# Kernel optimization log

Measured on AMD Instinct MI355X. Metric: run time of the kernel, lower is better.

## Reference

```python
import jax, jax.numpy as jnp
import numpy as np

CAUSAL = True


def setup_inputs() -> dict:
    key = jax.random.key(0)
    k1, k2, k3 = jax.random.split(key, 3)
    B, H, T, D = 2, 16, 2048, 64
    q = jax.random.normal(k1, (B, H, T, D), dtype=jnp.float32)
    k = jax.random.normal(k2, (B, H, T, D), dtype=jnp.float32)
    v = jax.random.normal(k3, (B, H, T, D), dtype=jnp.float32)
    return {"q": q, "k": k, "v": v}


def reference(q, k, v):
    # q,k,v: [B,H,T,D]
    d = q.shape[-1]
    scale = d ** -0.5
    dots = jnp.einsum('bhid,bhjd->bhij', q, k) * scale  # [B,H,T,T]
    if CAUSAL:
        t = q.shape[2]
        mask = jnp.triu(jnp.ones((t, t), dtype=bool), k=1)  # True above diagonal
        dots = jnp.where(mask, -jnp.inf, dots)
    attn = jax.nn.softmax(dots, axis=-1)
    # torch.einsum('bhjd,bhij->bhid', v, attn) == attn @ v
    return jnp.einsum('bhij,bhjd->bhid', attn, v)
```

## Files before the change

### kernel.cpp

```cpp
#include <hip/hip_runtime.h>
#include <hip/hip_bf16.h>

typedef unsigned short u16;
typedef unsigned int u32;
typedef __bf16 bf16x8 __attribute__((ext_vector_type(8)));
typedef short s16x4 __attribute__((ext_vector_type(4)));
typedef short s16x8 __attribute__((ext_vector_type(8)));
typedef float floatx4 __attribute__((ext_vector_type(4)));

#define T_SEQ 2048
#define HDIM 64
#define NBH 32

static __device__ __forceinline__ u16 f2b_rne(float x) {
    union { float f; u32 u; } c; c.f = x;
    u32 u = c.u;
    return (u16)((u + 0x7fffu + ((u >> 16) & 1u)) >> 16);
}
static __device__ __forceinline__ u16 f2b_trunc(float x) {
    union { float f; u32 u; } c; c.f = x;
    return (u16)(c.u >> 16);
}

#define GLOAD_LDS16(gp, lp)                                                      \
    __builtin_amdgcn_global_load_lds(                                            \
        (const __attribute__((address_space(1))) u32*)(gp),                      \
        (__attribute__((address_space(3))) u32*)(lp), 16, 0, 0)

__global__ __launch_bounds__(256) void prep(const float* __restrict__ k,
                                            const float* __restrict__ v,
                                            u16* __restrict__ kb,
                                            u16* __restrict__ vt) {
    __shared__ u16 tile[64][68];
    const int bh = blockIdx.y, t0 = blockIdx.x * 64;
    const int tid = threadIdx.x;

    const float* ksrc = k + ((size_t)bh * T_SEQ + t0) * HDIM;
    u16* kdst = kb + ((size_t)bh * T_SEQ + t0) * HDIM;
#pragma unroll
    for (int p = 0; p < 4; p++) {
        int idx = p * 256 + tid;
        float4 f = ((const float4*)ksrc)[idx];
        ushort4 o;
        o.x = f2b_rne(f.x); o.y = f2b_rne(f.y); o.z = f2b_rne(f.z); o.w = f2b_rne(f.w);
        ((ushort4*)kdst)[idx] = o;
    }

    const float* vsrc = v + ((size_t)bh * T_SEQ + t0) * HDIM;
#pragma unroll
    for (int p = 0; p < 4; p++) {
        int idx = p * 256 + tid;
        int r = idx >> 4, c4 = (idx & 15) * 4;
        float4 f = *(const float4*)(vsrc + r * HDIM + c4);
        tile[c4 + 0][r] = f2b_rne(f.x);
        tile[c4 + 1][r] = f2b_rne(f.y);
        tile[c4 + 2][r] = f2b_rne(f.z);
        tile[c4 + 3][r] = f2b_rne(f.w);
    }
    __syncthreads();
    u16* dst = vt + (size_t)bh * HDIM * T_SEQ + t0;
#pragma unroll
    for (int p = 0; p < 4; p++) {
        int idx = p * 256 + tid;
        int d = idx >> 4, c4 = (idx & 15) * 4;
        int t = c4 >> 4, qg = (c4 >> 2) & 3;
        int pos = qg * 16 + (t >> 1) * 8 + (t & 1) * 4;
        *(ushort4*)(dst + (size_t)d * T_SEQ + pos) = *(ushort4*)(&tile[d][c4]);
    }
}

__global__ __launch_bounds__(256, 4) void fattn(const float* __restrict__ q,
                                                const u16* __restrict__ kb,
                                                const u16* __restrict__ vtb,
                                                float* __restrict__ out) {
    __shared__ __align__(16) u16 Kl[2][64 * 64];
    __shared__ __align__(16) u16 Vl[2][64 * 64];

    const int bh = blockIdx.x;
    const int s = blockIdx.y;
    const int qt = (s & 8) ? (s ^ 7) : s;
    const int tid = threadIdx.x;
    const int wave = tid >> 6, lane = tid & 63;
    const int l15 = lane & 15, quad = lane >> 4;

    const float* qp = q + (size_t)bh * T_SEQ * HDIM;
    const u16* kp = kb + (size_t)bh * T_SEQ * HDIM;
    const u16* vp = vtb + (size_t)bh * HDIM * T_SEQ;

    const int qrow_base = qt * 64 + wave * 16;

    const int srow = wave * 8 + (lane >> 3);
    const int slot = lane & 7;
    const u16* kg0 = kp + srow * HDIM + (slot ^ (srow & 7)) * 8;
    const int vs = (slot - srow) & 7;
    const u16* vg0 = vp + (size_t)srow * T_SEQ + vs * 8;
    const u16* vg1 = vp + (size_t)(srow + 32) * T_SEQ + vs * 8;

    auto stage = [&](int j, int buf) {
        const u16* ks = kg0 + j * 64 * HDIM;
        u16* Kd = &Kl[buf][wave * 512];
        GLOAD_LDS16(ks, Kd);
        GLOAD_LDS16(ks + 32 * HDIM, Kd + 2048);
        u16* Vd = &Vl[buf][wave * 512];
        GLOAD_LDS16(vg0 + j * 64, Vd);
        GLOAD_LDS16(vg1 + j * 64, Vd + 2048);
    };

    stage(0, 0);

    const float SL2E = 0.125f * 1.44269504088896f;
    bf16x8 qf[2];
    {
        const float* qrow = qp + (size_t)(qrow_base + l15) * HDIM;
#pragma unroll
        for (int kc = 0; kc < 2; kc++) {
            const float4* p4 = (const float4*)(qrow + kc * 32 + quad * 8);
            float4 fa = p4[0], fb = p4[1];
            union { bf16x8 v; u16 s[8]; } cv;
            cv.s[0] = f2b_rne(fa.x * SL2E); cv.s[1] = f2b_rne(fa.y * SL2E);
            cv.s[2] = f2b_rne(fa.z * SL2E); cv.s[3] = f2b_rne(fa.w * SL2E);
            cv.s[4] = f2b_rne(fb.x * SL2E); cv.s[5] = f2b_rne(fb.y * SL2E);
            cv.s[6] = f2b_rne(fb.z * SL2E); cv.s[7] = f2b_rne(fb.w * SL2E);
            qf[kc] = cv.v;
        }
    }

    floatx4 o_acc[4];
#pragma unroll
    for (int dt = 0; dt < 4; dt++) o_acc[dt] = (floatx4){0.f, 0.f, 0.f, 0.f};
    float lsum = 0.f;

    for (int j = 0; j <= qt; ++j) {
        const int cur = j & 1;
        __syncthreads();

        if (j < qt) stage(j + 1, cur ^ 1);

        floatx4 sacc[4];
#pragma unroll
        for (int t = 0; t < 4; t++) sacc[t] = (floatx4){0.f, 0.f, 0.f, 0.f};
        const u16* Kc = Kl[cur];
#pragma unroll
        for (int kc = 0; kc < 2; kc++) {
#pragma unroll
            for (int t = 0; t < 4; t++) {
                int rk = t * 16 + l15;
                bf16x8 kf = *(const bf16x8*)(Kc + rk * 64 + ((kc * 4 + quad) ^ (rk & 7)) * 8);
                sacc[t] = __builtin_amdgcn_mfma_f32_16x16x32_bf16(kf, qf[kc], sacc[t], 0, 0, 0);
            }
        }

        s16x4 pfrag[4];
        const bool diag = (j == qt);
        const int gq = wave * 16 + l15;
#pragma unroll
        for (int t = 0; t < 4; t++) {
            union { s16x4 v; u16 h[4]; } pk;
#pragma unroll
            for (int rg = 0; rg < 4; rg++) {
                float e = __builtin_amdgcn_exp2f(sacc[t][rg]);
                if (diag && (t * 16 + quad * 4 + rg > gq)) e = 0.f;
                lsum += e;
                pk.h[rg] = f2b_trunc(e);
            }
            pfrag[t] = pk.v;
        }

        const u16* Vc = Vl[cur];
#pragma unroll
        for (int tp = 0; tp < 2; tp++) {
#pragma unroll
            for (int dt = 0; dt < 4; dt++) {
                int d = dt * 16 + l15;
                int sl = (quad * 2 + tp + d) & 7;
                s16x8 vf = *(const s16x8*)(Vc + d * 64 + sl * 8);
                s16x4 vf0 = __builtin_shufflevector(vf, vf, 0, 1, 2, 3);
                s16x4 vf1 = __builtin_shufflevector(vf, vf, 4, 5, 6, 7);
                o_acc[dt] = __builtin_amdgcn_mfma_f32_16x16x16bf16_1k(pfrag[2 * tp], vf0, o_acc[dt], 0, 0, 0);
                o_acc[dt] = __builtin_amdgcn_mfma_f32_16x16x16bf16_1k(pfrag[2 * tp + 1], vf1, o_acc[dt], 0, 0, 0);
            }
        }
    }

    float tot = lsum;
    tot += __shfl_xor(tot, 16, 64);
    tot += __shfl_xor(tot, 32, 64);
    float* op = out + (size_t)bh * T_SEQ * HDIM;
#pragma unroll
    for (int rg = 0; rg < 4; rg++) {
        float inv = 1.0f / __shfl(tot, quad * 4 + rg, 64);
        size_t row = (size_t)(qrow_base + quad * 4 + rg) * HDIM;
#pragma unroll
        for (int dt = 0; dt < 4; dt++)
            op[row + dt * 16 + l15] = o_acc[dt][rg] * inv;
    }
}

extern "C" void kernel_launch(void* const* d_in, const int* in_sizes, int n_in,
                              void* d_out, int out_size, void* d_ws, size_t ws_size,
                              hipStream_t stream) {
    const float* q = (const float*)d_in[0];
    const float* k = (const float*)d_in[1];
    const float* v = (const float*)d_in[2];
    float* out = (float*)d_out;

    u16* kb = (u16*)d_ws;
    u16* vt = kb + (size_t)NBH * T_SEQ * HDIM;

    prep<<<dim3(T_SEQ / 64, NBH), 256, 0, stream>>>(k, v, kb, vt);
    fattn<<<dim3(NBH, T_SEQ / 64), 256, 0, stream>>>(q, kb, vt, out);
}
```

Before: 123.7 us.

## Pair high and low causal query tiles in one 512-thread block sharing K/V stages

Result: no change. 123.5 us (-0.1%).

```diff
diff --git a/kernel.cpp b/kernel.cpp
--- a/kernel.cpp
+++ b/kernel.cpp
@@ -4,8 +4,7 @@
 typedef unsigned short u16;
 typedef unsigned int u32;
 typedef __bf16 bf16x8 __attribute__((ext_vector_type(8)));
-typedef short s16x4 __attribute__((ext_vector_type(4)));
-typedef short s16x8 __attribute__((ext_vector_type(8)));
+typedef u16 u16x8 __attribute__((ext_vector_type(8)));
 typedef float floatx4 __attribute__((ext_vector_type(4)));
 
 #define T_SEQ 2048
@@ -60,16 +59,18 @@
     __syncthreads();
     u16* dst = vt + (size_t)bh * HDIM * T_SEQ + t0;
 #pragma unroll
-    for (int p = 0; p < 4; p++) {
+    for (int p = 0; p < 2; p++) {
         int idx = p * 256 + tid;
-        int d = idx >> 4, c4 = (idx & 15) * 4;
-        int t = c4 >> 4, qg = (c4 >> 2) & 3;
-        int pos = qg * 16 + (t >> 1) * 8 + (t & 1) * 4;
-        *(ushort4*)(dst + (size_t)d * T_SEQ + pos) = *(ushort4*)(&tile[d][c4]);
-    }
-}
-
-__global__ __launch_bounds__(256, 4) void fattn(const float* __restrict__ q,
+        int d = idx >> 3, pb = idx & 7;
+        int k0 = (pb >> 2) * 32 + (pb & 3) * 4;
+        union { u16x8 v8; ushort4 q[2]; } w;
+        w.q[0] = *(ushort4*)&tile[d][k0];
+        w.q[1] = *(ushort4*)&tile[d][k0 + 16];
+        *(u16x8*)(dst + (size_t)d * T_SEQ + pb * 8) = w.v8;
+    }
+}
+
+__global__ __launch_bounds__(512, 4) void fattn(const float* __restrict__ q,
                                                 const u16* __restrict__ kb,
                                                 const u16* __restrict__ vtb,
                                                 float* __restrict__ out) {
@@ -78,32 +79,28 @@
 
     const int bh = blockIdx.x;
     const int s = blockIdx.y;
-    const int qt = (s & 8) ? (s ^ 7) : s;
+    const int pr = (s & 8) ? (s ^ 7) : s;
+    const int qtHi = 31 - pr, qtLo = pr;
+
     const int tid = threadIdx.x;
     const int wave = tid >> 6, lane = tid & 63;
     const int l15 = lane & 15, quad = lane >> 4;
+    const int qt = (wave < 4) ? qtHi : qtLo;
+    const int wrow = (wave & 3) * 16;
+    const int qrow_base = qt * 64 + wrow;
 
     const float* qp = q + (size_t)bh * T_SEQ * HDIM;
     const u16* kp = kb + (size_t)bh * T_SEQ * HDIM;
     const u16* vp = vtb + (size_t)bh * HDIM * T_SEQ;
 
-    const int qrow_base = qt * 64 + wave * 16;
-
     const int srow = wave * 8 + (lane >> 3);
     const int slot = lane & 7;
     const u16* kg0 = kp + srow * HDIM + (slot ^ (srow & 7)) * 8;
-    const int vs = (slot - srow) & 7;
-    const u16* vg0 = vp + (size_t)srow * T_SEQ + vs * 8;
-    const u16* vg1 = vp + (size_t)(srow + 32) * T_SEQ + vs * 8;
+    const u16* vg0 = vp + (size_t)srow * T_SEQ + ((slot - srow) & 7) * 8;
 
     auto stage = [&](int j, int buf) {
-        const u16* ks = kg0 + j * 64 * HDIM;
-        u16* Kd = &Kl[buf][wave * 512];
-        GLOAD_LDS16(ks, Kd);
-        GLOAD_LDS16(ks + 32 * HDIM, Kd + 2048);
-        u16* Vd = &Vl[buf][wave * 512];
-        GLOAD_LDS16(vg0 + j * 64, Vd);
-        GLOAD_LDS16(vg1 + j * 64, Vd + 2048);
+        GLOAD_LDS16(kg0 + j * 64 * HDIM, &Kl[buf][wave * 512]);
+        GLOAD_LDS16(vg0 + j * 64, &Vl[buf][wave * 512]);
     };
 
     stage(0, 0);
@@ -128,13 +125,14 @@
     floatx4 o_acc[4];
 #pragma unroll
     for (int dt = 0; dt < 4; dt++) o_acc[dt] = (floatx4){0.f, 0.f, 0.f, 0.f};
-    float lsum = 0.f;
-
-    for (int j = 0; j <= qt; ++j) {
+    float ls0 = 0.f, ls1 = 0.f;
+
+    for (int j = 0; j <= qtHi; ++j) {
         const int cur = j & 1;
         __syncthreads();
 
-        if (j < qt) stage(j + 1, cur ^ 1);
+        if (j < qtHi) stage(j + 1, cur ^ 1);
+        if (j > qt) continue;
 
         floatx4 sacc[4];
 #pragma unroll
@@ -150,20 +148,18 @@
             }
         }
 
-        s16x4 pfrag[4];
+        union { bf16x8 v; u16 h[8]; } pk[2];
         const bool diag = (j == qt);
-        const int gq = wave * 16 + l15;
+        const int gq = wrow + l15;
 #pragma unroll
         for (int t = 0; t < 4; t++) {
-            union { s16x4 v; u16 h[4]; } pk;
 #pragma unroll
             for (int rg = 0; rg < 4; rg++) {
                 float e = __builtin_amdgcn_exp2f(sacc[t][rg]);
                 if (diag && (t * 16 + quad * 4 + rg > gq)) e = 0.f;
-                lsum += e;
-                pk.h[rg] = f2b_trunc(e);
+                if (t < 2) ls0 += e; else ls1 += e;
+                pk[t >> 1].h[(t & 1) * 4 + rg] = f2b_trunc(e);
             }
-            pfrag[t] = pk.v;
         }
 
         const u16* Vc = Vl[cur];
@@ -172,17 +168,14 @@
 #pragma unroll
             for (int dt = 0; dt < 4; dt++) {
                 int d = dt * 16 + l15;
-                int sl = (quad * 2 + tp + d) & 7;
-                s16x8 vf = *(const s16x8*)(Vc + d * 64 + sl * 8);
-                s16x4 vf0 = __builtin_shufflevector(vf, vf, 0, 1, 2, 3);
-                s16x4 vf1 = __builtin_shufflevector(vf, vf, 4, 5, 6, 7);
-                o_acc[dt] = __builtin_amdgcn_mfma_f32_16x16x16bf16_1k(pfrag[2 * tp], vf0, o_acc[dt], 0, 0, 0);
-                o_acc[dt] = __builtin_amdgcn_mfma_f32_16x16x16bf16_1k(pfrag[2 * tp + 1], vf1, o_acc[dt], 0, 0, 0);
+                int sl = (tp * 4 + quad + d) & 7;
+                bf16x8 vf = *(const bf16x8*)(Vc + d * 64 + sl * 8);
+                o_acc[dt] = __builtin_amdgcn_mfma_f32_16x16x32_bf16(pk[tp].v, vf, o_acc[dt], 0, 0, 0);
             }
         }
     }
 
-    float tot = lsum;
+    float tot = ls0 + ls1;
     tot += __shfl_xor(tot, 16, 64);
     tot += __shfl_xor(tot, 32, 64);
     float* op = out + (size_t)bh * T_SEQ * HDIM;
@@ -208,5 +201,5 @@
     u16* vt = kb + (size_t)NBH * T_SEQ * HDIM;
 
     prep<<<dim3(T_SEQ / 64, NBH), 256, 0, stream>>>(k, v, kb, vt);
-    fattn<<<dim3(NBH, T_SEQ / 64), 256, 0, stream>>>(q, kb, vt, out);
-}
+    fattn<<<dim3(NBH, 16), 512, 0, stream>>>(q, kb, vt, out);
+}
```
